# Kernel tuning notes

Measured on AMD Instinct MI355X. Metric: run time of the kernel, lower is better.

## Reference

```python
import jax, jax.numpy as jnp
import numpy as np
from jax import lax

V = 50000          # vocab
E = 64             # embedding_dim
B = 64             # batch
SEQ = 1024         # sentence length
NC = 6             # num_classes
L = 4              # num_layers (total conv layers)
KTOP = 4
NF = [10, 14, 18, 22]          # num_filters per stage
KS = [7, 5, 5, 3]              # kernel sizes
ROWS = [E // 2**i for i in range(5)]   # [64,32,16,8,4]
GROUPS = ROWS[:4]              # conv_i groups = rows[i-1]
# dynamic k-max schedule: k_l = max(k_top, ceil((L-l)/L * SEQ)) for l=1,2,3; last pool uses k_top
KPOOL = [max(KTOP, int(np.ceil((L - l) / L * SEQ))) for l in (1, 2, 3)] + [KTOP]  # [768,512,256,4]


def _uniform(key, shape, fan):
    s = 1.0 / np.sqrt(fan)
    return jax.random.uniform(key, shape, jnp.float32, -s, s)


def setup_inputs() -> dict:
    key = jax.random.key(0)
    ks = jax.random.split(key, 16)
    tokens = jax.random.randint(ks[0], (B, SEQ), 0, V)
    emb = jax.random.normal(ks[1], (V, E), jnp.float32)
    inp = {"tokens": tokens, "emb": emb}
    # conv weights: OIH layout, I = in_channels / groups = num_filters[i-1] (or 1 for conv1)
    in_pg = [1, NF[0], NF[1], NF[2]]
    out_ch = [NF[i] * ROWS[i] for i in range(4)]   # [640,448,288,176]
    for i in range(4):
        fan = in_pg[i] * KS[i]
        inp[f"w{i+1}"] = _uniform(ks[2 + 2 * i], (out_ch[i], in_pg[i], KS[i]), fan)
        inp[f"b{i+1}"] = _uniform(ks[3 + 2 * i], (out_ch[i],), fan)
    fc_in = ROWS[4] * NF[3] * KTOP   # 4*22*4 = 352
    inp["fcw"] = _uniform(ks[10], (NC, fc_in), fc_in)
    inp["fcb"] = _uniform(ks[11], (NC,), fc_in)
    return inp


def _fold(x, nf):
    # channel index c = row*nf + filt; sum adjacent rows pairwise (Fold(2,2))
    b, d, s = x.shape
    r = d // nf
    return x.reshape(b, r // 2, 2, nf, s).sum(axis=2).reshape(b, d // 2, s)


def _kmax(x, k):
    # top-k along seq axis, preserving original temporal order
    _, idx = lax.top_k(x, k)
    idx = jnp.sort(idx, axis=-1)
    return jnp.take_along_axis(x, idx, axis=-1)


def reference(tokens, emb, w1, b1, w2, b2, w3, b3, w4, b4, fcw, fcb):
    x = emb[tokens]                 # (B, S, E)
    x = x.transpose(0, 2, 1)        # (B, E, S)
    ws, bs = (w1, w2, w3, w4), (b1, b2, b3, b4)
    for i in range(4):
        pad = KS[i] - 1             # 'wide' convolution
        x = lax.conv_general_dilated(
            x, ws[i], (1,), [(pad, pad)],
            dimension_numbers=("NCH", "OIH", "NCH"),
            feature_group_count=GROUPS[i],
        ) + bs[i][None, :, None]
        x = _fold(x, NF[i])
        x = _kmax(x, KPOOL[i])
        x = jnp.tanh(x)
    # dropout is identity in eval mode
    x = x.reshape(x.shape[0], -1)   # (B, 352)
    return x @ fcw.T + fcb
```

## Files before the change

kernel.cpp:

```cpp
#include <hip/hip_runtime.h>
#include <hip/hip_bf16.h>
#include <math.h>


#if defined(__has_builtin)
#if __has_builtin(__builtin_amdgcn_ballot_w64)
#define BALLOT64(expr) __builtin_amdgcn_ballot_w64(expr)
#endif
#endif
#ifndef BALLOT64
#define BALLOT64(expr) __ballot(expr)
#endif

__device__ __forceinline__ unsigned f2ord(float f) {
    unsigned u = __float_as_uint(f);
    return (u & 0x80000000u) ? ~u : (u | 0x80000000u);
}
__device__ __forceinline__ float ord2f(unsigned key) {
    unsigned u = (key & 0x80000000u) ? (key & 0x7fffffffu) : ~key;
    return __uint_as_float(u);
}
__device__ __forceinline__ float tanh_fast(float x) {
    float e = __expf(2.f * x);
    return 1.f - 2.f * __builtin_amdgcn_rcpf(e + 1.f);
}
__device__ __forceinline__ int mbcnt64(unsigned long long m) {
    return __builtin_amdgcn_mbcnt_hi((unsigned)(m >> 32),
           __builtin_amdgcn_mbcnt_lo((unsigned)m, 0u));
}

template<int CH, bool COPY>
__device__ __forceinline__ void select_finish(const unsigned* keys, unsigned T,
                                              int k, float* stage,
                                              float* __restrict__ out)
{
    int g = 0, e = 0;
    #pragma unroll
    for (int i = 0; i < CH; ++i) { g += (keys[i] > T); e += (keys[i] == T); }

    int gtBefore = 0, eqBefore = 0, totG = 0;
    #pragma unroll
    for (int b = 0; b < 5; ++b) {
        unsigned long long mg = BALLOT64((((g >> b) & 1) != 0));
        unsigned long long me = BALLOT64((((e >> b) & 1) != 0));
        gtBefore += mbcnt64(mg) << b;
        eqBefore += mbcnt64(me) << b;
        totG     += __popcll(mg) << b;
    }
    const int needTies = k - totG;

    int gRun = 0, eRun = 0;
    #pragma unroll
    for (int i = 0; i < CH; ++i) {
        const unsigned key = keys[i];
        const bool isG = key > T;
        const bool isE = key == T;
        const int eIdx = eqBefore + eRun;
        const int dst = gtBefore + gRun + min(eIdx, needTies);
        if (isG || (isE && eIdx < needTies))
            stage[dst] = tanh_fast(ord2f(key));
        gRun += isG; eRun += isE;
    }
    if (COPY) {
        const int lane = threadIdx.x & 63;
        const float4* s4 = (const float4*)stage;
        float4* o4 = (float4*)out;
        #pragma unroll 1
        for (int i = lane; i < (k >> 2); i += 64)
            o4[i] = s4[i];
    }
}

template<int CH, bool COPY>
__device__ void wave_select1(const unsigned* keys, int k, float* stage,
                             float* __restrict__ out)
{
    unsigned p = 0u;
    int above = 0, buck = 64 * CH;
    #pragma unroll 1
    for (int pos = 31; pos >= 0; --pos) {
        const unsigned t = p | (1u << pos);
        int c = 0;
        #pragma unroll
        for (int i = 0; i < CH; ++i)
            c += __popcll(BALLOT64((keys[i] >= t)));
        const int inb = c - above;
        const int rem = k - above;
        if (inb >= rem) { p = t; buck = inb; }
        else            { above += inb; buck -= inb; }
        if (buck == k - above) break;
    }
    select_finish<CH, COPY>(keys, p, k, stage, out);
}

template<int N, int CH>
__device__ void wave_selectN_ballot(const unsigned (*keys)[CH], int k,
                                    float* stage, float* const* outs)
{
    unsigned p[N];
    int above[N], buck[N];
    #pragma unroll
    for (int n = 0; n < N; ++n) { p[n] = 0u; above[n] = 0; buck[n] = 64 * CH; }

    unsigned doneMask = 0;
    const unsigned allDone = (1u << N) - 1u;
    #pragma unroll 1
    for (int pos = 31; pos >= 0; --pos) {
        #pragma unroll
        for (int n = 0; n < N; ++n) {
            if (!((doneMask >> n) & 1u)) {
                const unsigned t = p[n] | (1u << pos);
                int c = 0;
                #pragma unroll
                for (int i = 0; i < CH; ++i)
                    c += __popcll(BALLOT64((keys[n][i] >= t)));
                const int inb = c - above[n];
                const int rem = k - above[n];
                if (inb >= rem) { p[n] = t; buck[n] = inb; }
                else            { above[n] += inb; buck[n] -= inb; }
                if (buck[n] == k - above[n]) doneMask |= (1u << n);
            }
        }
        if (doneMask == allDone) break;
    }
    #pragma unroll
    for (int n = 0; n < N; ++n)
        select_finish<CH, true>(keys[n], p[n], k, stage, outs[n]);
}

__global__ __launch_bounds__(896) void layer12_fused(
    const int* __restrict__ tokens, const float* __restrict__ emb,
    const float* __restrict__ W1, const float* __restrict__ B1,
    const float* __restrict__ W2, const float* __restrict__ B2,
    float* __restrict__ Z2)
{
    const int j2 = blockIdx.x;
    const int b  = blockIdx.y;
    const int t  = threadIdx.x;
    const int wav  = t >> 6;
    const int lane = t & 63;

    __shared__ __align__(16) float z1[10][836];
    __shared__ __align__(16) float uni[14 * 512];
    float (*xr)[1100] = reinterpret_cast<float (*)[1100]>(uni);
    const float2* emb2 = (const float2*)emb;

    for (int i = t; i < 10 * 836; i += 896) ((float*)z1)[i] = 0.f;

    const int f = __builtin_amdgcn_readfirstlane(wav);
    float acc[13];
    {
        const float bias = B2[(2 * j2) * 14 + f] + B2[(2 * j2 + 1) * 14 + f];
        #pragma unroll
        for (int i = 0; i < 13; ++i) acc[i] = bias;
    }
    const int base = lane * 13;

    {
        const int g = 2 * j2;
        for (int i = t; i < 1100; i += 896) {
            int s = i - 6; float a = 0.f, c = 0.f;
            if (s >= 0 && s < 1024) {
                int tok = tokens[b * 1024 + s];
                float2 v = emb2[(size_t)tok * 32 + g];
                a = v.x; c = v.y;
            }
            xr[0][i] = a; xr[1][i] = c;
        }
    }
    __syncthreads();

    #pragma unroll 1
    for (int ph = 0; ph < 2; ++ph) {
        const int g = 2 * j2 + ph;

        if (wav < 10) {
            const int f1 = wav;
            float wa[7], wb[7];
            #pragma unroll
            for (int k2 = 0; k2 < 7; ++k2) {
                wa[k2] = W1[(2 * g * 10 + f1) * 7 + k2];
                wb[k2] = W1[((2 * g + 1) * 10 + f1) * 7 + k2];
            }
            const float bias1 = B1[2 * g * 10 + f1] + B1[(2 * g + 1) * 10 + f1];
            const int beg = lane * 17;
            unsigned keys1[17];
            #pragma unroll
            for (int i = 0; i < 17; ++i) {
                float a1 = bias1;
                #pragma unroll
                for (int k2 = 0; k2 < 7; ++k2)
                    a1 += xr[0][beg + i + k2] * wa[k2]
                        + xr[1][beg + i + k2] * wb[k2];
                keys1[i] = (beg + i < 1030) ? f2ord(a1) : 0u;
            }
            wave_select1<17, false>(keys1, 768, &z1[wav][4], nullptr);
        }
        __syncthreads();

        if (ph == 0) {
            const int g1 = 2 * j2 + 1;
            for (int i = t; i < 1100; i += 896) {
                int s = i - 6; float a = 0.f, c = 0.f;
                if (s >= 0 && s < 1024) {
                    int tok = tokens[b * 1024 + s];
                    float2 v = emb2[(size_t)tok * 32 + g1];
                    a = v.x; c = v.y;
                }
                xr[0][i] = a; xr[1][i] = c;
            }
        }

        {
            const float* Wp0 = W2 + (size_t)((2 * j2 + ph) * 14 + f) * 10 * 5;
            #pragma unroll 1
            for (int r = 0; r < 10; ++r) {
                float win[17];
                #pragma unroll
                for (int p = 0; p < 17; ++p) win[p] = z1[r][base + p];
                const float* Wp = Wp0 + r * 5;
                #pragma unroll
                for (int k2 = 0; k2 < 5; ++k2) {
                    const float w0 = Wp[k2];
                    #pragma unroll
                    for (int i = 0; i < 13; ++i)
                        acc[i] = fmaf(win[i + k2], w0, acc[i]);
                }
            }
        }
        if (ph == 0) __syncthreads();
    }

    unsigned keys2[13];
    #pragma unroll
    for (int i = 0; i < 13; ++i)
        keys2[i] = (base + i < 772) ? f2ord(acc[i]) : 0u;
    float* stage = uni + wav * 512;
    float* outp = Z2 + ((size_t)b * 224 + (size_t)j2 * 14 + f) * 512;
    wave_select1<13, true>(keys2, 512, stage, outp);
}

template <int IPG, int NF, int K, int SIN, int SOUT, int KSEL, int NW, int CH,
          int PHASES>
__global__ __launch_bounds__(NW * 64) void conv_fold_select_kernel(
    const float* __restrict__ X, const float* __restrict__ W,
    const float* __restrict__ Bias, float* __restrict__ Z,
    int Cin, int Cfold)
{
    static_assert(NF == 2 * NW, "2 filters per wave");
    static_assert(64 * CH >= SOUT, "chunk covers row");
    constexpr int W2 = 64 * CH + K - 1;
    constexpr int RS = 2 * IPG / PHASES;

    const int t = threadIdx.x;
    const int j = blockIdx.x;
    const int b = blockIdx.y;
    const int wav = t >> 6, lane = t & 63;

    __shared__ __align__(16) float xs[RS][W2];
    __shared__ __align__(16) float stagebuf[NW][KSEL];

    const float* Xb = X + ((size_t)b * Cin + (size_t)(2 * j) * IPG) * SIN;

    const int f0 = __builtin_amdgcn_readfirstlane(2 * wav);
    float acc0[CH], acc1[CH];
    {
        float bias0 = Bias[2 * j * NF + f0]     + Bias[(2 * j + 1) * NF + f0];
        float bias1 = Bias[2 * j * NF + f0 + 1] + Bias[(2 * j + 1) * NF + f0 + 1];
        #pragma unroll
        for (int i = 0; i < CH; ++i) { acc0[i] = bias0; acc1[i] = bias1; }
    }
    const int base = lane * CH;

    #pragma unroll 1
    for (int ph = 0; ph < PHASES; ++ph) {
        if (ph) __syncthreads();
        for (int idx = t; idx < RS * W2; idx += NW * 64) {
            int r = idx / W2, p = idx - r * W2;
            int sg = p - (K - 1);
            int gr = ph * RS + r;
            xs[r][p] = (sg >= 0 && sg < SIN) ? Xb[(size_t)gr * SIN + sg] : 0.f;
        }
        __syncthreads();

        int h = (ph * RS) / IPG, c = (ph * RS) % IPG;
        #pragma unroll 1
        for (int r = 0; r < RS; ++r) {
            float win[CH + K - 1];
            #pragma unroll
            for (int p = 0; p < CH + K - 1; ++p)
                win[p] = xs[r][base + p];
            const float* Wp = W + ((size_t)((2 * j + h) * NF + f0) * IPG + c) * K;
            #pragma unroll
            for (int k2 = 0; k2 < K; ++k2) {
                const float w0 = Wp[k2];
                const float w1 = Wp[(size_t)IPG * K + k2];
                #pragma unroll
                for (int i = 0; i < CH; ++i) {
                    acc0[i] = fmaf(win[i + k2], w0, acc0[i]);
                    acc1[i] = fmaf(win[i + k2], w1, acc1[i]);
                }
            }
            if (++c == IPG) { c = 0; ++h; }
        }
    }

    unsigned keys[2][CH];
    #pragma unroll
    for (int i = 0; i < CH; ++i) {
        keys[0][i] = (base + i < SOUT) ? f2ord(acc0[i]) : 0u;
        keys[1][i] = (base + i < SOUT) ? f2ord(acc1[i]) : 0u;
    }
    const size_t orow = (size_t)b * Cfold + (size_t)j * NF;
    float* outs[2] = { Z + (orow + f0) * (size_t)KSEL,
                       Z + (orow + f0 + 1) * (size_t)KSEL };
    wave_selectN_ballot<2, CH>(keys, KSEL, stagebuf[wav], outs);
}

__global__ __launch_bounds__(192) void fc_kernel(
    const float* __restrict__ Z, const float* __restrict__ Wf,
    const float* __restrict__ bf, float* __restrict__ out)
{
    int g = blockIdx.x * blockDim.x + threadIdx.x;
    if (g >= 64 * 6) return;
    int b = g / 6, c = g % 6;
    float acc = bf[c];
    const float* zr = Z + b * 352;
    const float* wr = Wf + c * 352;
    for (int i = 0; i < 352; ++i) acc += zr[i] * wr[i];
    out[g] = acc;
}

extern "C" void kernel_launch(void* const* d_in, const int* in_sizes, int n_in,
                              void* d_out, int out_size, void* d_ws, size_t ws_size,
                              hipStream_t stream)
{
    const int*   tokens = (const int*)  d_in[0];
    const float* emb    = (const float*)d_in[1];
    const float* w1     = (const float*)d_in[2];
    const float* b1     = (const float*)d_in[3];
    const float* w2     = (const float*)d_in[4];
    const float* b2     = (const float*)d_in[5];
    const float* w3     = (const float*)d_in[6];
    const float* b3     = (const float*)d_in[7];
    const float* w4     = (const float*)d_in[8];
    const float* b4     = (const float*)d_in[9];
    const float* fcw    = (const float*)d_in[10];
    const float* fcb    = (const float*)d_in[11];
    float* out = (float*)d_out;
    float* ws  = (float*)d_ws;

    float* Z2 = ws + 15728640;
    float* Z3 = ws;
    float* Z4 = ws + 2359296;

    layer12_fused<<<dim3(16, 64), 896, 0, stream>>>(
        tokens, emb, w1, b1, w2, b2, Z2);

    conv_fold_select_kernel<14, 18, 5, 512, 516, 256, 9, 9, 1>
        <<<dim3(8, 64), 9 * 64, 0, stream>>>(Z2, w3, b3, Z3, 224, 144);

    conv_fold_select_kernel<18, 22, 3, 256, 258, 4, 11, 5, 1>
        <<<dim3(4, 64), 11 * 64, 0, stream>>>(Z3, w4, b4, Z4, 144, 88);

    fc_kernel<<<2, 192, 0, stream>>>(Z4, fcw, fcb, out);
}
```

Baseline: 331.0 us.

## Batch layer-1 threshold search for both groups with DPP wave reductions

Loads the embedding rows for both layer-1 groups into shared memory at once and computes both conv outputs up front. It then runs a single interleaved radix threshold search over both groups, replacing per-bit ballot/popcount counting with lane-local counts and a DPP wave sum. The layer-2 accumulation is split into two unrolled passes with a select_finish between them. This removes one embedding reload, shares the search loop's latency across two independent selections, and should shorten the serial chain. In exchange it holds 34 keys per lane in registers, which raises register pressure at 896 threads per block.

```diff
diff --git a/kernel.cpp b/kernel.cpp
--- a/kernel.cpp
+++ b/kernel.cpp
@@ -27,6 +27,16 @@
 __device__ __forceinline__ int mbcnt64(unsigned long long m) {
     return __builtin_amdgcn_mbcnt_hi((unsigned)(m >> 32),
            __builtin_amdgcn_mbcnt_lo((unsigned)m, 0u));
+}
+
+__device__ __forceinline__ int wave_sum64(int v) {
+    v += __builtin_amdgcn_update_dpp(0, v, 0x111, 0xf, 0xf, true);
+    v += __builtin_amdgcn_update_dpp(0, v, 0x112, 0xf, 0xf, true);
+    v += __builtin_amdgcn_update_dpp(0, v, 0x114, 0xf, 0xf, true);
+    v += __builtin_amdgcn_update_dpp(0, v, 0x118, 0xf, 0xf, true);
+    v += __builtin_amdgcn_update_dpp(0, v, 0x142, 0xa, 0xf, false);
+    v += __builtin_amdgcn_update_dpp(0, v, 0x143, 0xc, 0xf, false);
+    return __builtin_amdgcn_readlane(v, 63);
 }
 
 template<int CH, bool COPY>
@@ -71,6 +81,45 @@
     }
 }
 
+template<int N, int CH>
+__device__ void wave_searchN_dpp(const unsigned (*keys)[CH], int k,
+                                 unsigned* pOut)
+{
+    unsigned p[N];
+    int above[N], buck[N];
+    #pragma unroll
+    for (int n = 0; n < N; ++n) { p[n] = 0u; above[n] = 0; buck[n] = 64 * CH; }
+
+    unsigned doneMask = 0;
+    const unsigned allDone = (1u << N) - 1u;
+    #pragma unroll 1
+    for (int pos = 31; pos >= 0; --pos) {
+        #pragma unroll
+        for (int n = 0; n < N; ++n) {
+            if (!((doneMask >> n) & 1u)) {
+                const unsigned t = p[n] | (1u << pos);
+                int c0 = 0, c1 = 0, c2 = 0, c3 = 0;
+                #pragma unroll
+                for (int i = 0; i < CH; i += 4) {
+                    c0 += (keys[n][i] >= t);
+                    if (i + 1 < CH) c1 += (keys[n][i + 1] >= t);
+                    if (i + 2 < CH) c2 += (keys[n][i + 2] >= t);
+                    if (i + 3 < CH) c3 += (keys[n][i + 3] >= t);
+                }
+                const int c = wave_sum64((c0 + c1) + (c2 + c3));
+                const int inb = c - above[n];
+                const int rem = k - above[n];
+                if (inb >= rem) { p[n] = t; buck[n] = inb; }
+                else            { above[n] += inb; buck[n] -= inb; }
+                if (buck[n] == k - above[n]) doneMask |= (1u << n);
+            }
+        }
+        if (doneMask == allDone) break;
+    }
+    #pragma unroll
+    for (int n = 0; n < N; ++n) pOut[n] = p[n];
+}
+
 template<int CH, bool COPY>
 __device__ void wave_select1(const unsigned* keys, int k, float* stage,
                              float* __restrict__ out)
@@ -142,7 +191,7 @@
 
     __shared__ __align__(16) float z1[10][836];
     __shared__ __align__(16) float uni[14 * 512];
-    float (*xr)[1100] = reinterpret_cast<float (*)[1100]>(uni);
+    float (*xr)[2][1100] = reinterpret_cast<float (*)[2][1100]>(uni);
     const float2* emb2 = (const float2*)emb;
 
     for (int i = t; i < 10 * 836; i += 896) ((float*)z1)[i] = 0.f;
@@ -156,26 +205,27 @@
     }
     const int base = lane * 13;
 
-    {
-        const int g = 2 * j2;
-        for (int i = t; i < 1100; i += 896) {
-            int s = i - 6; float a = 0.f, c = 0.f;
-            if (s >= 0 && s < 1024) {
-                int tok = tokens[b * 1024 + s];
-                float2 v = emb2[(size_t)tok * 32 + g];
-                a = v.x; c = v.y;
-            }
-            xr[0][i] = a; xr[1][i] = c;
-        }
+    for (int i = t; i < 2200; i += 896) {
+        const int g01 = i / 1100;
+        const int p = i - g01 * 1100;
+        const int s = p - 6;
+        float a = 0.f, c = 0.f;
+        if (s >= 0 && s < 1024) {
+            int tok = tokens[b * 1024 + s];
+            float2 v = emb2[(size_t)tok * 32 + 2 * j2 + g01];
+            a = v.x; c = v.y;
+        }
+        xr[g01][0][p] = a; xr[g01][1][p] = c;
     }
     __syncthreads();
 
-    #pragma unroll 1
-    for (int ph = 0; ph < 2; ++ph) {
-        const int g = 2 * j2 + ph;
-
-        if (wav < 10) {
-            const int f1 = wav;
+    unsigned keys1[2][17];
+    unsigned T1[2];
+    if (wav < 10) {
+        const int f1 = wav;
+        #pragma unroll
+        for (int g01 = 0; g01 < 2; ++g01) {
+            const int g = 2 * j2 + g01;
             float wa[7], wb[7];
             #pragma unroll
             for (int k2 = 0; k2 < 7; ++k2) {
@@ -184,51 +234,60 @@
             }
             const float bias1 = B1[2 * g * 10 + f1] + B1[(2 * g + 1) * 10 + f1];
             const int beg = lane * 17;
-            unsigned keys1[17];
             #pragma unroll
             for (int i = 0; i < 17; ++i) {
                 float a1 = bias1;
                 #pragma unroll
                 for (int k2 = 0; k2 < 7; ++k2)
-                    a1 += xr[0][beg + i + k2] * wa[k2]
-                        + xr[1][beg + i + k2] * wb[k2];
-                keys1[i] = (beg + i < 1030) ? f2ord(a1) : 0u;
-            }
-            wave_select1<17, false>(keys1, 768, &z1[wav][4], nullptr);
-        }
-        __syncthreads();
-
-        if (ph == 0) {
-            const int g1 = 2 * j2 + 1;
-            for (int i = t; i < 1100; i += 896) {
-                int s = i - 6; float a = 0.f, c = 0.f;
-                if (s >= 0 && s < 1024) {
-                    int tok = tokens[b * 1024 + s];
-                    float2 v = emb2[(size_t)tok * 32 + g1];
-                    a = v.x; c = v.y;
-                }
-                xr[0][i] = a; xr[1][i] = c;
-            }
-        }
-
-        {
-            const float* Wp0 = W2 + (size_t)((2 * j2 + ph) * 14 + f) * 10 * 5;
-            #pragma unroll 1
-            for (int r = 0; r < 10; ++r) {
-                float win[17];
-                #pragma unroll
-                for (int p = 0; p < 17; ++p) win[p] = z1[r][base + p];
-                const float* Wp = Wp0 + r * 5;
-                #pragma unroll
-                for (int k2 = 0; k2 < 5; ++k2) {
-                    const float w0 = Wp[k2];
-                    #pragma unroll
-                    for (int i = 0; i < 13; ++i)
-                        acc[i] = fmaf(win[i + k2], w0, acc[i]);
-                }
-            }
-        }
-        if (ph == 0) __syncthreads();
+                    a1 += xr[g01][0][beg + i + k2] * wa[k2]
+                        + xr[g01][1][beg + i + k2] * wb[k2];
+                keys1[g01][i] = (beg + i < 1030) ? f2ord(a1) : 0u;
+            }
+        }
+        wave_searchN_dpp<2, 17>(keys1, 768, T1);
+        select_finish<17, false>(keys1[0], T1[0], 768, &z1[wav][4], nullptr);
+    }
+    __syncthreads();
+
+    {
+        const float* Wp0 = W2 + (size_t)((2 * j2) * 14 + f) * 10 * 5;
+        #pragma unroll 1
+        for (int r = 0; r < 10; ++r) {
+            float win[17];
+            #pragma unroll
+            for (int p = 0; p < 17; ++p) win[p] = z1[r][base + p];
+            const float* Wp = Wp0 + r * 5;
+            #pragma unroll
+            for (int k2 = 0; k2 < 5; ++k2) {
+                const float w0 = Wp[k2];
+                #pragma unroll
+                for (int i = 0; i < 13; ++i)
+                    acc[i] = fmaf(win[i + k2], w0, acc[i]);
+            }
+        }
+    }
+    __syncthreads();
+
+    if (wav < 10)
+        select_finish<17, false>(keys1[1], T1[1], 768, &z1[wav][4], nullptr);
+    __syncthreads();
+
+    {
+        const float* Wp0 = W2 + (size_t)((2 * j2 + 1) * 14 + f) * 10 * 5;
+        #pragma unroll 1
+        for (int r = 0; r < 10; ++r) {
+            float win[17];
+            #pragma unroll
+            for (int p = 0; p < 17; ++p) win[p] = z1[r][base + p];
+            const float* Wp = Wp0 + r * 5;
+            #pragma unroll
+            for (int k2 = 0; k2 < 5; ++k2) {
+                const float w0 = Wp[k2];
+                #pragma unroll
+                for (int i = 0; i < 13; ++i)
+                    acc[i] = fmaf(win[i + k2], w0, acc[i]);
+            }
+        }
     }
 
     unsigned keys2[13];
```

Result: slower. 346.7 us (+4.7%).
